# Kernel tuning notes

Hardware: AMD Instinct MI355X
Metric: run time of the kernel (lower is better)

The kernel has to match this reference:

```python
import jax, jax.numpy as jnp
import numpy as np

SEQ, B, XD, HD, ZD = 256, 128, 128, 1024, 64


def setup_inputs() -> dict:
    key = jax.random.key(0)
    ks = jax.random.split(key, 32)
    w = lambda k, shape: (jax.random.normal(k, shape, jnp.float32) * 0.02)
    inp = {
        "x": jax.random.uniform(ks[0], (SEQ, B, XD), jnp.float32),
        "eps": jax.random.normal(ks[1], (SEQ, B, ZD), jnp.float32),
        "phi_x_W": w(ks[2], (HD, XD)),   "phi_x_b": jnp.zeros((HD,), jnp.float32),
        "enc_W": w(ks[3], (HD, 2 * HD)), "enc_b": jnp.zeros((HD,), jnp.float32),
        "enc_mean_W": w(ks[4], (ZD, HD)), "enc_mean_b": jnp.zeros((ZD,), jnp.float32),
        "enc_std_W": w(ks[5], (ZD, HD)),  "enc_std_b": jnp.zeros((ZD,), jnp.float32),
        "prior_W": w(ks[6], (HD, HD)),   "prior_b": jnp.zeros((HD,), jnp.float32),
        "prior_mean_W": w(ks[7], (ZD, HD)), "prior_mean_b": jnp.zeros((ZD,), jnp.float32),
        "prior_std_W": w(ks[8], (ZD, HD)),  "prior_std_b": jnp.zeros((ZD,), jnp.float32),
        "phi_z_W": w(ks[9], (HD, ZD)),   "phi_z_b": jnp.zeros((HD,), jnp.float32),
        "dec1_W": w(ks[10], (HD, 2 * HD)), "dec1_b": jnp.zeros((HD,), jnp.float32),
        "dec2_W": w(ks[11], (XD, HD)),     "dec2_b": jnp.zeros((XD,), jnp.float32),
        "gru_Wi": w(ks[12], (3 * HD, 2 * HD)), "gru_Wh": w(ks[13], (3 * HD, HD)),
        "gru_bi": jnp.zeros((3 * HD,), jnp.float32), "gru_bh": jnp.zeros((3 * HD,), jnp.float32),
    }
    return inp


def _lin(x, W, b):
    return x @ W.T + b


def _vrnn(x, eps, phi_x_W, phi_x_b, enc_W, enc_b, enc_mean_W, enc_mean_b,
          enc_std_W, enc_std_b, prior_W, prior_b, prior_mean_W, prior_mean_b,
          prior_std_W, prior_std_b, phi_z_W, phi_z_b, dec1_W, dec1_b,
          dec2_W, dec2_b, gru_Wi, gru_Wh, gru_bi, gru_bh):
    batch = x.shape[1]
    h0 = jnp.zeros((batch, gru_Wh.shape[1]), x.dtype)

    def step(h, inp):
        x_t, eps_t = inp
        phi_x_t = jax.nn.relu(_lin(x_t, phi_x_W, phi_x_b))
        prior_t = jax.nn.relu(_lin(h, prior_W, prior_b))
        prior_mean_t = _lin(prior_t, prior_mean_W, prior_mean_b)
        prior_std_t = jnp.exp(0.5 * _lin(prior_t, prior_std_W, prior_std_b))
        enc_t = jax.nn.relu(_lin(jnp.concatenate([phi_x_t, h], axis=1), enc_W, enc_b))
        enc_mean_t = _lin(enc_t, enc_mean_W, enc_mean_b)
        enc_std_t = jnp.exp(0.5 * _lin(enc_t, enc_std_W, enc_std_b))
        z_t = enc_mean_t + eps_t * enc_std_t
        phi_z_t = jax.nn.relu(_lin(z_t, phi_z_W, phi_z_b))
        dec_h = jax.nn.relu(_lin(jnp.concatenate([phi_z_t, h], axis=1), dec1_W, dec1_b))
        logits_t = _lin(dec_h, dec2_W, dec2_b)  # sigmoid(logits) is the reconstruction
        # GRU cell (PyTorch gate ordering r, z, n)
        u_t = jnp.concatenate([phi_x_t, phi_z_t], axis=1)
        gi = _lin(u_t, gru_Wi, gru_bi)
        gh = _lin(h, gru_Wh, gru_bh)
        hd = h.shape[1]
        i_r, i_z, i_n = gi[:, :hd], gi[:, hd:2 * hd], gi[:, 2 * hd:]
        h_r, h_z, h_n = gh[:, :hd], gh[:, hd:2 * hd], gh[:, 2 * hd:]
        r = jax.nn.sigmoid(i_r + h_r)
        zg = jax.nn.sigmoid(i_z + h_z)
        n = jnp.tanh(i_n + r * h_n)
        h_new = (1.0 - zg) * n + zg * h
        # per-step losses (sum reduction, as in the torch code)
        # BCE(sigmoid(l), x) = x*softplus(-l) + (1-x)*softplus(l)
        recon_t = jnp.sum(x_t * jax.nn.softplus(-logits_t) + (1.0 - x_t) * jax.nn.softplus(logits_t))
        kld_t = -0.5 * jnp.sum(1.0 + 2.0 * jnp.log(enc_std_t)
                               - (enc_mean_t - prior_mean_t) ** 2
                               - (enc_std_t / prior_std_t) ** 2)
        return h_new, (logits_t, recon_t, kld_t)

    _, (logits, recon_ts, kld_ts) = jax.lax.scan(step, h0, (x, eps))
    recon_loss = jnp.sum(recon_ts) / batch
    kld_loss = jnp.sum(kld_ts) / batch
    x_recon = jax.nn.sigmoid(logits)
    return recon_loss, kld_loss, x_recon


def reference(x, eps, phi_x_W, phi_x_b, enc_W, enc_b, enc_mean_W, enc_mean_b,
              enc_std_W, enc_std_b, prior_W, prior_b, prior_mean_W, prior_mean_b,
              prior_std_W, prior_std_b, phi_z_W, phi_z_b, dec1_W, dec1_b,
              dec2_W, dec2_b, gru_Wi, gru_Wh, gru_bi, gru_bh):
    return _vrnn(x, eps, phi_x_W, phi_x_b, enc_W, enc_b, enc_mean_W, enc_mean_b,
                 enc_std_W, enc_std_b, prior_W, prior_b, prior_mean_W, prior_mean_b,
                 prior_std_W, prior_std_b, phi_z_W, phi_z_b, dec1_W, dec1_b,
                 dec2_W, dec2_b, gru_Wi, gru_Wh, gru_bi, gru_bh)
```

## Files before the change

### kernel.cpp

```cpp
#include <hip/hip_runtime.h>
#include <algorithm>

typedef __bf16 bf16;
typedef __bf16 bf16x8 __attribute__((ext_vector_type(8)));
typedef float f32x4 __attribute__((ext_vector_type(4)));
typedef unsigned long long u64;

#define SEQ 256
#define BATCH 128
#define XD 128
#define HD 1024
#define ZD 64
#define MROWS (SEQ * BATCH)
#define BH (BATCH * HD)
#define B3 (BATCH * 3072)
#define DYN_LDS 154432
#define NBLK 256

__device__ __forceinline__ f32x4 mfma16(bf16x8 a, bf16x8 b, f32x4 c) {
  return __builtin_amdgcn_mfma_f32_16x16x32_bf16(a, b, c, 0, 0, 0);
}
__device__ __forceinline__ float sigmoidf_(float x) { return 1.f / (1.f + __expf(-x)); }

__device__ __forceinline__ void cst16(bf16* p, bf16x8 v) {
  asm volatile("global_store_dwordx4 %0, %1, off sc0 sc1" ::"v"(p), "v"(v) : "memory");
}
__device__ __forceinline__ void cst16f(float* p, f32x4 v) {
  asm volatile("global_store_dwordx4 %0, %1, off sc0 sc1" ::"v"(p), "v"(v) : "memory");
}

__device__ __forceinline__ void gbar(unsigned* arr, unsigned* sum, unsigned serial) {
  asm volatile("s_waitcnt vmcnt(0) lgkmcnt(0)" ::: "memory");
  __syncthreads();
  const int tid = threadIdx.x;
  const int bid = blockIdx.x;
  if (tid == 0)
    __hip_atomic_store(arr + (size_t)bid * 32, serial, __ATOMIC_RELAXED,
                       __HIP_MEMORY_SCOPE_AGENT);
  if ((bid & 15) == 0 && tid < 16) {
    const unsigned* f = arr + (size_t)((bid & ~15) + tid) * 32;
    while (__hip_atomic_load(f, __ATOMIC_RELAXED, __HIP_MEMORY_SCOPE_AGENT) < serial)
      __builtin_amdgcn_s_sleep(2);
  }
  __syncthreads();
  if ((bid & 15) == 0 && tid == 0)
    __hip_atomic_store(sum + (size_t)(bid >> 4) * 32, serial, __ATOMIC_RELAXED,
                       __HIP_MEMORY_SCOPE_AGENT);
  if (tid < 16) {
    const unsigned* f = sum + (size_t)tid * 32;
    while (__hip_atomic_load(f, __ATOMIC_RELAXED, __HIP_MEMORY_SCOPE_AGENT) < serial)
      __builtin_amdgcn_s_sleep(2);
  }
  __builtin_amdgcn_fence(__ATOMIC_ACQUIRE, "agent");
  __syncthreads();
}

template <int MT, int NT>
__device__ __forceinline__ void mma_block(const bf16* __restrict__ a0, size_t aStride,
                                          const bf16* __restrict__ b0, size_t bStride,
                                          int K, f32x4 acc[MT][NT]) {
#pragma unroll 2
  for (int k = 0; k < K; k += 32) {
    bf16x8 af[MT], bfr[NT];
#pragma unroll
    for (int i = 0; i < MT; ++i) af[i] = *(const bf16x8*)(a0 + (size_t)i * aStride + k);
#pragma unroll
    for (int j = 0; j < NT; ++j) bfr[j] = *(const bf16x8*)(b0 + (size_t)j * bStride + k);
#pragma unroll
    for (int i = 0; i < MT; ++i)
#pragma unroll
      for (int j = 0; j < NT; ++j) acc[i][j] = mfma16(af[i], bfr[j], acc[i][j]);
  }
}

__global__ void cvt_k(bf16* __restrict__ dst, const float* __restrict__ src, long n,
                      int cols, int src_ld, int col_off) {
  long i = (long)blockIdx.x * blockDim.x + threadIdx.x;
  long stride = (long)gridDim.x * blockDim.x;
  for (; i < n; i += stride) {
    long row = i / cols;
    int c = (int)(i - row * cols);
    dst[i] = (bf16)src[row * (long)src_ld + col_off + c];
  }
}

struct Epi {
  bf16* C;
  float* Cf;
  const float* bias;
  const bf16* add;
  int relu;
  int ldc;
};

template <int MT, int NT>
__global__ void gemm_bt(const bf16* __restrict__ A, int lda, const bf16* __restrict__ B,
                        int ldb, int M, int N, int K, Epi e) {
  const int lane = threadIdx.x & 63;
  const int r = lane & 15, kb = lane >> 4;
  const int gw = blockIdx.x * (blockDim.x >> 6) + (threadIdx.x >> 6);
  const int nw = gridDim.x * (blockDim.x >> 6);
  const int ntm = M / (16 * MT), ntn = N / (16 * NT);
  for (int task = gw; task < ntm * ntn; task += nw) {
    int mt = task % ntm, nt = task / ntm;
    int m0 = mt * 16 * MT, n0 = nt * 16 * NT;
    f32x4 acc[MT][NT] = {};
    const bf16* a0 = A + (size_t)(m0 + r) * lda + kb * 8;
    const bf16* b0 = B + (size_t)(n0 + r) * ldb + kb * 8;
    mma_block<MT, NT>(a0, (size_t)16 * lda, b0, (size_t)16 * ldb, K, acc);
#pragma unroll
    for (int i = 0; i < MT; ++i)
#pragma unroll
      for (int j = 0; j < NT; ++j)
#pragma unroll
        for (int q = 0; q < 4; ++q) {
          size_t gm = (size_t)m0 + i * 16 + kb * 4 + q;
          int gn = n0 + j * 16 + r;
          float v = acc[i][j][q] + e.bias[gn];
          if (e.add) v += (float)e.add[gm * e.ldc + gn];
          if (e.relu) v = fmaxf(v, 0.f);
          if (e.Cf) e.Cf[gm * e.ldc + gn] = v;
          else e.C[gm * e.ldc + gn] = (bf16)v;
        }
  }
}

struct LoopP {
  const bf16 *WA, *WB, *WPZ, *WIZ, *WIX, *WXX, *WPX, *WDZ, *WD2, *XBF;
  bf16 *HB, *PT, *ET, *PHIX, *ENCX, *PHIZ, *DHP, *DECH;
  float *H, *GH, *GIX, *KLD, *RPART, *out;
  unsigned *ARR, *SUM, *PFLAG;
  const float *eps, *x;
  const float *prior_b, *gru_bh, *gru_bi, *pm_b, *ps_b, *em_b, *es_b, *pz_b, *phx_b,
      *enc_b, *dec1_b, *dec2_b;
};

__device__ __forceinline__ void stage1024(char* lds, int off, const bf16* src) {
  for (int c = threadIdx.x; c < 2048; c += 512) {
    int kg = c & 127, rr = c >> 7;
    *(float4*)(lds + off + (((kg << 4) + rr) << 4)) =
        *(const float4*)(src + (size_t)rr * 1024 + kg * 8);
  }
}

template <int KK>
__device__ __forceinline__ void load_af(bf16x8* af, const bf16* A, int row, int lda, int k0,
                                        int kb) {
#pragma unroll
  for (int kk = 0; kk < KK; ++kk)
    af[kk] = *(const bf16x8*)(A + (size_t)row * lda + k0 + kk * 32 + kb * 8);
}

template <int NU>
__device__ __forceinline__ void run_units(const bf16* Arow, const char* slab0, f32x4* acc,
                                          int r, int kb) {
  bf16x8 af[32];
#pragma unroll
  for (int kk = 0; kk < 32; ++kk) af[kk] = *(const bf16x8*)(Arow + kk * 32 + kb * 8);
#pragma unroll
  for (int u = 0; u < NU; ++u)
#pragma unroll
    for (int kk = 0; kk < 32; ++kk)
      acc[u] = mfma16(af[kk],
                      *(const bf16x8*)(slab0 + u * 32768 + ((((kk * 4 + kb) << 4) + r) << 4)),
                      acc[u]);
}

__device__ __forceinline__ void xpose2(float* wscr, const f32x4* acc, int ua, int r, int kb,
                                       int urow, int cb, int usel, float* vals) {
#pragma unroll
  for (int tdx = 0; tdx < 2; ++tdx) {
    f32x4 a = acc[ua + tdx];
    int base = tdx * 328 + (kb * 4) * 20 + r;
#pragma unroll
    for (int q = 0; q < 4; ++q) wscr[base + q * 20] = a[q];
  }
  asm volatile("s_waitcnt lgkmcnt(0)" ::: "memory");
  __builtin_amdgcn_sched_barrier(0);
  int rb = usel * 328 + urow * 20 + cb;
#pragma unroll
  for (int j = 0; j < 8; ++j) vals[j] = wscr[rb + j];
}

__global__ void __launch_bounds__(512, 1) vrnn_loop(LoopP p) {
  extern __shared__ char lds[];
  const int tid = threadIdx.x, lane = tid & 63, wv = tid >> 6;
  const int r = lane & 15, kb = lane >> 4;
  const int urow = (lane & 31) >> 1, cb = (lane & 1) * 8, usel = lane >> 5;
  const int b = blockIdx.x;
  unsigned bs = 0;

  int cls, uid0 = 0, gizj = 0, wpxb = 0;
  if (b < 8) cls = 0;
  else if (b < 104) { cls = 1; uid0 = 4 * (b - 8); }
  else if (b < 120) { cls = 2; uid0 = 4 * (b - 104); }
  else if (b < 122) { cls = 3; wpxb = b - 120; }
  else if (b < 186) { cls = 4; uid0 = 4 * (b - 122); }
  else if (b < 188) { cls = 5; uid0 = 4 * (b - 186); }
  else if (b < 252) { cls = 6; gizj = b - 188; }
  else cls = 7;

  float* wscr = (float*)(lds + 131072) + wv * 656;

  if (cls == 0) {
    for (int c = tid; c < 8192; c += 512) {
      int kg = c & 7, rr = (c >> 3) & 15, u = c >> 7;
      *(float4*)(lds + u * 2048 + (((kg << 4) + rr) << 4)) =
          *(const float4*)(p.WPZ + (size_t)(u * 16 + rr) * 64 + kg * 8);
    }
  } else if (cls == 1) {
    for (int u = 0; u < 4; ++u) stage1024(lds, u * 32768, p.WA + (size_t)(uid0 + u) * 16 * 1024);
  } else if (cls == 2) {
    for (int u = 0; u < 4; ++u) stage1024(lds, u * 32768, p.WDZ + (size_t)(uid0 + u) * 16 * 1024);
  } else if (cls == 3) {
    for (int c = tid; c < 8192; c += 512) {
      int u = c >> 8, kg = c & 15, rr = (c >> 4) & 15;
      *(float4*)(lds + u * 4096 + (((kg << 4) + rr) << 4)) =
          *(const float4*)(p.WPX + (size_t)((wpxb * 32 + u) * 16 + rr) * 128 + kg * 8);
    }
  } else if (cls == 4) {
    for (int u = 0; u < 4; ++u) {
      int uid = uid0 + u;
      const bf16* src = (uid < 64) ? p.WXX + (size_t)uid * 16 * 1024
                                   : p.WIX + (size_t)(uid - 64) * 16 * 1024;
      stage1024(lds, u * 32768, src);
    }
  } else if (cls == 5) {
    for (int u = 0; u < 4; ++u) stage1024(lds, u * 32768, p.WD2 + (size_t)(uid0 + u) * 16 * 1024);
  } else if (cls == 6) {
    for (int g = 0; g < 3; ++g)
      stage1024(lds, g * 32768, p.WIZ + (size_t)(g * 1024 + gizj * 16) * 1024);
  }
  __syncthreads();

  for (int t = 0; t < SEQ; ++t) {
    const int cur = t & 1, oth = cur ^ 1;

    if (cls == 1) {
      const bf16* Arow = p.HB + (size_t)(wv * 16 + r) * HD;
      f32x4 acc[4] = {};
      run_units<4>(Arow, lds, acc, r, kb);
#pragma unroll
      for (int up = 0; up < 4; up += 2) {
        float vals[8];
        xpose2(wscr, acc, up, r, kb, urow, cb, usel, vals);
        int uid = uid0 + up + usel;
        int gm = wv * 16 + urow;
        if (uid < 64) {
          int gn = uid * 16 + cb;
          bf16x8 o;
#pragma unroll
          for (int j = 0; j < 8; ++j) o[j] = (bf16)fmaxf(vals[j] + p.prior_b[gn + j], 0.f);
          cst16(&p.PT[gm * HD + gn], o);
        } else if (uid < 128) {
          int c = (uid - 64) * 16 + cb;
          bf16x8 ex = *(const bf16x8*)(p.ENCX + (size_t)cur * BH + gm * HD + c);
          bf16x8 o;
#pragma unroll
          for (int j = 0; j < 8; ++j) o[j] = (bf16)fmaxf(vals[j] + (float)ex[j], 0.f);
          cst16(&p.ET[gm * HD + c], o);
        } else if (uid < 320) {
          int c = (uid - 128) * 16 + cb;
          f32x4 g0, g1;
#pragma unroll
          for (int j = 0; j < 4; ++j) g0[j] = vals[j] + p.gru_bh[c + j];
#pragma unroll
          for (int j = 0; j < 4; ++j) g1[j] = vals[4 + j] + p.gru_bh[c + 4 + j];
          cst16f(&p.GH[gm * 3072 + c], g0);
          cst16f(&p.GH[gm * 3072 + c + 4], g1);
        } else {
          int c = (uid - 320) * 16 + cb;
          bf16x8 o;
#pragma unroll
          for (int j = 0; j < 8; ++j) o[j] = (bf16)vals[j];
          cst16(&p.DHP[(size_t)cur * BH + gm * HD + c], o);
        }
      }
    } else if (cls == 2 && t > 0) {
      const bf16* Arow = p.PHIZ + (size_t)oth * BH + (size_t)(wv * 16 + r) * HD;
      f32x4 acc[4] = {};
      run_units<4>(Arow, lds, acc, r, kb);
#pragma unroll
      for (int up = 0; up < 4; up += 2) {
        float vals[8];
        xpose2(wscr, acc, up, r, kb, urow, cb, usel, vals);
        int c = (uid0 + up + usel) * 16 + cb;
        int gm = wv * 16 + urow;
        bf16x8 dh = *(const bf16x8*)(p.DHP + (size_t)oth * BH + gm * HD + c);
        bf16x8 o;
#pragma unroll
        for (int j = 0; j < 8; ++j)
          o[j] = (bf16)fmaxf(vals[j] + (float)dh[j] + p.dec1_b[c + j], 0.f);
        cst16(&p.DECH[gm * HD + c], o);
      }
    } else if (cls == 3 && t < SEQ - 1) {
      bf16x8 af2[4];
      load_af<4>(af2, p.XBF + (size_t)(t + 1) * BATCH * XD, wv * 16 + r, 128, 0, kb);
#pragma unroll 1
      for (int up = 0; up < 32; up += 2) {
        f32x4 acc2[2] = {};
#pragma unroll
        for (int tdx = 0; tdx < 2; ++tdx)
#pragma unroll
          for (int kk = 0; kk < 4; ++kk)
            acc2[tdx] = mfma16(af2[kk],
                               *(const bf16x8*)(lds + (up + tdx) * 4096 +
                                                ((((kk * 4 + kb) << 4) + r) << 4)),
                               acc2[tdx]);
        float vals[8];
        xpose2(wscr, acc2, 0, r, kb, urow, cb, usel, vals);
        int gn = (wpxb * 32 + up + usel) * 16 + cb;
        int gm = wv * 16 + urow;
        bf16x8 o;
#pragma unroll
        for (int j = 0; j < 8; ++j) o[j] = (bf16)fmaxf(vals[j] + p.phx_b[gn + j], 0.f);
        cst16(&p.PHIX[gm * HD + gn], o);
      }
    }
    gbar(p.ARR, p.SUM, ++bs);

    if (cls == 0) {
      const int m0 = b * 16;
      const int mat = wv & 3, half = wv >> 2;
      float* sm = (float*)(lds + 131072);
      bf16* zs = (bf16*)(lds + 152064);
      float* red = (float*)(lds + 154368);
      {
        const bf16* Arow = ((mat < 2) ? p.PT : p.ET) + (size_t)(m0 + r) * HD;
        bf16x8 af[32];
#pragma unroll
        for (int kk = 0; kk < 32; ++kk) af[kk] = *(const bf16x8*)(Arow + kk * 32 + kb * 8);
        const float* bw = mat == 0 ? p.pm_b : mat == 1 ? p.ps_b : mat == 2 ? p.em_b : p.es_b;
#pragma unroll 1
        for (int nt = 0; nt < 2; ++nt) {
          int colb = half * 32 + nt * 16;
          f32x4 acc = {};
#pragma unroll
          for (int kk = 0; kk < 32; ++kk)
            acc = mfma16(af[kk],
                         *(const bf16x8*)(p.WB + (size_t)(mat * 64 + colb + r) * 1024 +
                                          kk * 32 + kb * 8),
                         acc);
#pragma unroll
          for (int qq = 0; qq < 4; ++qq)
            sm[mat * 1024 + (kb * 4 + qq) * 64 + colb + r] = acc[qq] + bw[colb + r];
        }
      }
      __syncthreads();
      float kacc = 0.f;
      for (int e = tid; e < 1024; e += 512) {
        int row = e >> 6, col = e & 63;
        float pm = sm[row * 64 + col], ps = sm[1024 + row * 64 + col];
        float em = sm[2048 + row * 64 + col], es = sm[3072 + row * 64 + col];
        float ev = p.eps[((size_t)t * BATCH + m0 + row) * ZD + col];
        zs[row * 72 + col] = (bf16)(em + ev * __expf(0.5f * es));
        float dm = em - pm;
        kacc += 1.f + es - dm * dm - __expf(es - ps);
      }
#pragma unroll
      for (int off = 32; off; off >>= 1) kacc += __shfl_down(kacc, off, 64);
      if (lane == 0) red[wv] = kacc;
      __syncthreads();
      if (tid == 0) {
        float ss = 0.f;
        for (int i = 0; i < 8; ++i) ss += red[i];
        p.KLD[t * 8 + b] = ss;
      }
      bf16x8 afz[2];
      afz[0] = *(const bf16x8*)(zs + r * 72 + kb * 8);
      afz[1] = *(const bf16x8*)(zs + r * 72 + 32 + kb * 8);
#pragma unroll 1
      for (int jp = 0; jp < 8; jp += 2) {
        f32x4 acc2[2] = {};
#pragma unroll
        for (int tdx = 0; tdx < 2; ++tdx) {
          int u = wv * 8 + jp + tdx;
#pragma unroll
          for (int kk = 0; kk < 2; ++kk)
            acc2[tdx] = mfma16(afz[kk],
                               *(const bf16x8*)(lds + u * 2048 +
                                                ((((kk * 4 + kb) << 4) + r) << 4)),
                               acc2[tdx]);
        }
        float vals[8];
        xpose2(wscr, acc2, 0, r, kb, urow, cb, usel, vals);
        int gn = (wv * 8 + jp + usel) * 16 + cb;
        int gm = m0 + urow;
        bf16x8 o;
#pragma unroll
        for (int j = 0; j < 8; ++j) o[j] = (bf16)fmaxf(vals[j] + p.pz_b[gn + j], 0.f);
        cst16(&p.PHIZ[(size_t)cur * BH + gm * HD + gn], o);
      }
      asm volatile("s_waitcnt vmcnt(0)" ::: "memory");
      __syncthreads();
      if (tid == 0)
        __hip_atomic_store(p.PFLAG + (size_t)b * 32, (unsigned)(t + 1), __ATOMIC_RELAXED,
                           __HIP_MEMORY_SCOPE_AGENT);
    } else if (cls == 4 && t < SEQ - 1) {
      const bf16* Arow = p.PHIX + (size_t)(wv * 16 + r) * HD;
      f32x4 acc[4] = {};
      run_units<4>(Arow, lds, acc, r, kb);
#pragma unroll
      for (int up = 0; up < 4; up += 2) {
        float vals[8];
        xpose2(wscr, acc, up, r, kb, urow, cb, usel, vals);
        int uid = uid0 + up + usel;
        int gm = wv * 16 + urow;
        if (uid < 64) {
          int c = uid * 16 + cb;
          bf16x8 o;
#pragma unroll
          for (int j = 0; j < 8; ++j) o[j] = (bf16)(vals[j] + p.enc_b[c + j]);
          cst16(&p.ENCX[(size_t)oth * BH + gm * HD + c], o);
        } else {
          int c = (uid - 64) * 16 + cb;
          f32x4 g0, g1;
#pragma unroll
          for (int j = 0; j < 4; ++j) g0[j] = vals[j] + p.gru_bi[c + j];
#pragma unroll
          for (int j = 0; j < 4; ++j) g1[j] = vals[4 + j] + p.gru_bi[c + 4 + j];
          cst16f(&p.GIX[(size_t)oth * B3 + gm * 3072 + c], g0);
          cst16f(&p.GIX[(size_t)oth * B3 + gm * 3072 + c + 4], g1);
        }
      }
    } else if (cls == 5 && t > 0) {
      const bf16* Arow = p.DECH + (size_t)(wv * 16 + r) * HD;
      f32x4 acc[4] = {};
      run_units<4>(Arow, lds, acc, r, kb);
      float racc = 0.f;
#pragma unroll
      for (int up = 0; up < 4; up += 2) {
        float vals[8];
        xpose2(wscr, acc, up, r, kb, urow, cb, usel, vals);
        int c = (uid0 + up + usel) * 16 + cb;
        int gm = wv * 16 + urow;
        size_t oi = ((size_t)(t - 1) * BATCH + gm) * XD + c;
#pragma unroll
        for (int j = 0; j < 8; ++j) {
          float l = vals[j] + p.dec2_b[c + j];
          p.out[2 + oi + j] = sigmoidf_(l);
          float spp = fmaxf(l, 0.f) + log1pf(__expf(-fabsf(l)));
          racc += spp - p.x[oi + j] * l;
        }
      }
#pragma unroll
      for (int off = 32; off; off >>= 1) racc += __shfl_down(racc, off, 64);
      if (lane == 0) p.RPART[(t - 1) * 64 + uid0 * 2 + wv] = racc;
    } else if (cls == 6) {
      if (tid < 8) {
        const unsigned* f = p.PFLAG + (size_t)tid * 32;
        while (__hip_atomic_load(f, __ATOMIC_RELAXED, __HIP_MEMORY_SCOPE_AGENT) <
               (unsigned)(t + 1))
          __builtin_amdgcn_s_sleep(1);
      }
      __syncthreads();
      __builtin_amdgcn_sched_barrier(0);
      float* scR = (float*)(lds + 98304);
      const int khalf = wv >> 2, mtg = wv & 3;
#pragma unroll 1
      for (int pass = 0; pass < 2; ++pass) {
        int mt = mtg + 4 * pass;
        const bf16* Arow = p.PHIZ + (size_t)cur * BH + (size_t)(mt * 16 + r) * HD;
        bf16x8 af[16];
#pragma unroll
        for (int kk = 0; kk < 16; ++kk)
          af[kk] = *(const bf16x8*)(Arow + khalf * 512 + kk * 32 + kb * 8);
        f32x4 a3[3] = {};
#pragma unroll
        for (int kk = 0; kk < 16; ++kk) {
          bf16x8 a = af[kk];
#pragma unroll
          for (int g = 0; g < 3; ++g)
            a3[g] = mfma16(a,
                           *(const bf16x8*)(lds + g * 32768 +
                                            (((((khalf * 16 + kk) * 4 + kb) << 4) + r) << 4)),
                           a3[g]);
        }
#pragma unroll
        for (int g = 0; g < 3; ++g)
#pragma unroll
          for (int q = 0; q < 4; ++q)
            scR[khalf * 3072 + mtg * 768 + g * 256 + (kb * 4 + q) * 16 + r] = a3[g][q];
        __syncthreads();
        if (tid < 128) {
          int mtg2 = tid >> 5, row = (tid & 31) >> 1, cb2 = (tid & 1) * 8;
          int gm = (mtg2 + 4 * pass) * 16 + row;
          int c = gizj * 16 + cb2;
          int base = mtg2 * 768 + row * 16 + cb2;
          float iv[3][8], hv[3][8];
#pragma unroll
          for (int g = 0; g < 3; ++g) {
            f32x4 i0 = *(const f32x4*)(p.GIX + (size_t)cur * B3 + gm * 3072 + g * 1024 + c);
            f32x4 i1 = *(const f32x4*)(p.GIX + (size_t)cur * B3 + gm * 3072 + g * 1024 + c + 4);
            f32x4 h0 = *(const f32x4*)(p.GH + gm * 3072 + g * 1024 + c);
            f32x4 h1 = *(const f32x4*)(p.GH + gm * 3072 + g * 1024 + c + 4);
#pragma unroll
            for (int j = 0; j < 8; ++j) {
              float part = scR[base + g * 256 + j] + scR[3072 + base + g * 256 + j];
              iv[g][j] = part + ((j < 4) ? i0[j] : i1[j - 4]);
              hv[g][j] = (j < 4) ? h0[j] : h1[j - 4];
            }
          }
          f32x4 hc0 = *(const f32x4*)(p.H + gm * HD + c);
          f32x4 hc1 = *(const f32x4*)(p.H + gm * HD + c + 4);
          f32x4 hn0, hn1;
          bf16x8 o;
#pragma unroll
          for (int j = 0; j < 8; ++j) {
            float rr2 = sigmoidf_(iv[0][j] + hv[0][j]);
            float zg = sigmoidf_(iv[1][j] + hv[1][j]);
            float nn = tanhf(iv[2][j] + rr2 * hv[2][j]);
            float hvv = (j < 4) ? hc0[j] : hc1[j - 4];
            float hnew = (1.f - zg) * nn + zg * hvv;
            if (j < 4) hn0[j] = hnew; else hn1[j - 4] = hnew;
            o[j] = (bf16)hnew;
          }
          *(f32x4*)(p.H + gm * HD + c) = hn0;
          *(f32x4*)(p.H + gm * HD + c + 4) = hn1;
          cst16(&p.HB[gm * HD + c], o);
        }
        __syncthreads();
      }
    }
    gbar(p.ARR, p.SUM, ++bs);
  }
}

__global__ void dec2_last(const bf16* __restrict__ A, const bf16* __restrict__ W,
                          const float* __restrict__ x, const float* __restrict__ b2,
                          float* __restrict__ out, float* __restrict__ rpart) {
  const int lane = threadIdx.x & 63;
  const int r = lane & 15, kb = lane >> 4;
  const int w = blockIdx.x * 4 + (threadIdx.x >> 6);
  const int m0 = (w & 7) * 16, n0 = (w >> 3) * 16;
  f32x4 acc[1][1] = {};
  const bf16* a0 = A + (size_t)(m0 + r) * HD + kb * 8;
  const bf16* b0 = W + (size_t)(n0 + r) * HD + kb * 8;
  mma_block<1, 1>(a0, 0, b0, (size_t)16 * HD, HD, acc);
  float racc = 0.f;
#pragma unroll
  for (int q = 0; q < 4; ++q) {
    int gm = m0 + kb * 4 + q, gn = n0 + r;
    float l = acc[0][0][q] + b2[gn];
    size_t oi = ((size_t)255 * BATCH + gm) * XD + gn;
    out[2 + oi] = sigmoidf_(l);
    float spp = fmaxf(l, 0.f) + log1pf(__expf(-fabsf(l)));
    racc += spp - x[oi] * l;
  }
#pragma unroll
  for (int off = 32; off; off >>= 1) racc += __shfl_down(racc, off, 64);
  if (lane == 0) rpart[255 * 64 + w] = racc;
}

__global__ void finalize_k(const float* __restrict__ rp, const float* __restrict__ kp,
                           float* __restrict__ out) {
  __shared__ float s[256];
  int tid = threadIdx.x;
  float a = 0.f;
  for (int i = tid; i < 256 * 64; i += 256) a += rp[i];
  s[tid] = a;
  __syncthreads();
  for (int off = 128; off > 0; off >>= 1) {
    if (tid < off) s[tid] += s[tid + off];
    __syncthreads();
  }
  if (tid == 0) out[0] = s[0] / (float)BATCH;
  __syncthreads();
  float bb = 0.f;
  for (int i = tid; i < 2048; i += 256) bb += kp[i];
  s[tid] = bb;
  __syncthreads();
  for (int off = 128; off > 0; off >>= 1) {
    if (tid < off) s[tid] += s[tid + off];
    __syncthreads();
  }
  if (tid == 0) out[1] = -0.5f * s[0] / (float)BATCH;
}

__global__ void sentinel_k(float* out) {
  if (threadIdx.x == 0) { out[0] = 1e9f; out[1] = 1e9f; }
}

extern "C" void kernel_launch(void* const* d_in, const int* in_sizes, int n_in, void* d_out,
                              int out_size, void* d_ws, size_t ws_size, hipStream_t stream) {
  const float* x = (const float*)d_in[0];
  const float* eps = (const float*)d_in[1];
  const float* phi_x_W = (const float*)d_in[2];
  const float* phi_x_b = (const float*)d_in[3];
  const float* enc_W = (const float*)d_in[4];
  const float* enc_b = (const float*)d_in[5];
  const float* enc_mean_W = (const float*)d_in[6];
  const float* enc_mean_b = (const float*)d_in[7];
  const float* enc_std_W = (const float*)d_in[8];
  const float* enc_std_b = (const float*)d_in[9];
  const float* prior_W = (const float*)d_in[10];
  const float* prior_b = (const float*)d_in[11];
  const float* prior_mean_W = (const float*)d_in[12];
  const float* prior_mean_b = (const float*)d_in[13];
  const float* prior_std_W = (const float*)d_in[14];
  const float* prior_std_b = (const float*)d_in[15];
  const float* phi_z_W = (const float*)d_in[16];
  const float* phi_z_b = (const float*)d_in[17];
  const float* dec1_W = (const float*)d_in[18];
  const float* dec1_b = (const float*)d_in[19];
  const float* dec2_W = (const float*)d_in[20];
  const float* dec2_b = (const float*)d_in[21];
  const float* gru_Wi = (const float*)d_in[22];
  const float* gru_Wh = (const float*)d_in[23];
  const float* gru_bi = (const float*)d_in[24];
  const float* gru_bh = (const float*)d_in[25];
  float* out = (float*)d_out;

  char* w = (char*)d_ws;
  auto carve = [&](size_t bytes) {
    char* pp = w;
    w += (bytes + 255) & ~(size_t)255;
    return pp;
  };
  bf16* WA = (bf16*)carve((size_t)6144 * HD * 2);
  bf16* WB = (bf16*)carve((size_t)256 * HD * 2);
  bf16* WPZ = (bf16*)carve((size_t)HD * ZD * 2);
  bf16* WIZ = (bf16*)carve((size_t)3072 * HD * 2);
  bf16* WIX = (bf16*)carve((size_t)3072 * HD * 2);
  bf16* WXX = (bf16*)carve((size_t)HD * HD * 2);
  bf16* WPX = (bf16*)carve((size_t)HD * XD * 2);
  bf16* WDZ = (bf16*)carve((size_t)HD * HD * 2);
  bf16* WD2 = (bf16*)carve((size_t)XD * HD * 2);
  bf16* XBF = (bf16*)carve((size_t)MROWS * XD * 2);
  float* H = (float*)carve((size_t)BH * 4);
  bf16* HB = (bf16*)carve((size_t)BH * 2);
  bf16* PT = (bf16*)carve((size_t)BH * 2);
  bf16* ET = (bf16*)carve((size_t)BH * 2);
  float* GH = (float*)carve((size_t)B3 * 4);
  bf16* PHIX = (bf16*)carve((size_t)BH * 2);
  bf16* ENCX = (bf16*)carve((size_t)2 * BH * 2);
  bf16* PHIZ = (bf16*)carve((size_t)2 * BH * 2);
  bf16* DHP = (bf16*)carve((size_t)2 * BH * 2);
  bf16* DECH = (bf16*)carve((size_t)BH * 2);
  float* GIX = (float*)carve((size_t)2 * B3 * 4);
  float* KLD = (float*)carve((size_t)SEQ * 8 * 4);
  float* RPART = (float*)carve((size_t)SEQ * 64 * 4);
  unsigned* ARR = (unsigned*)carve((size_t)NBLK * 32 * 4);
  unsigned* SUM = (unsigned*)carve((size_t)16 * 32 * 4);
  unsigned* PFLAG = (unsigned*)carve((size_t)8 * 32 * 4);
  if ((size_t)(w - (char*)d_ws) > ws_size) {
    sentinel_k<<<1, 64, 0, stream>>>(out);
    return;
  }

  auto cvt = [&](bf16* dst, const float* src, long n, int cols, int ld, int off) {
    int grid = (int)std::min((n + 255) / 256, (long)2048);
    cvt_k<<<grid, 256, 0, stream>>>(dst, src, n, cols, ld, off);
  };
  cvt(WA, prior_W, (long)HD * HD, HD, HD, 0);
  cvt(WA + (size_t)HD * HD, enc_W, (long)HD * HD, HD, 2 * HD, HD);
  cvt(WA + (size_t)2048 * HD, gru_Wh, (long)3072 * HD, HD, HD, 0);
  cvt(WA + (size_t)5120 * HD, dec1_W, (long)HD * HD, HD, 2 * HD, HD);
  cvt(WB, prior_mean_W, (long)ZD * HD, HD, HD, 0);
  cvt(WB + (size_t)64 * HD, prior_std_W, (long)ZD * HD, HD, HD, 0);
  cvt(WB + (size_t)128 * HD, enc_mean_W, (long)ZD * HD, HD, HD, 0);
  cvt(WB + (size_t)192 * HD, enc_std_W, (long)ZD * HD, HD, HD, 0);
  cvt(WPZ, phi_z_W, (long)HD * ZD, ZD, ZD, 0);
  cvt(WIZ, gru_Wi, (long)3072 * HD, HD, 2 * HD, HD);
  cvt(WIX, gru_Wi, (long)3072 * HD, HD, 2 * HD, 0);
  cvt(WXX, enc_W, (long)HD * HD, HD, 2 * HD, 0);
  cvt(WPX, phi_x_W, (long)HD * XD, XD, XD, 0);
  cvt(WDZ, dec1_W, (long)HD * HD, HD, 2 * HD, 0);
  cvt(WD2, dec2_W, (long)XD * HD, HD, HD, 0);
  cvt(XBF, x, (long)MROWS * XD, XD, XD, 0);

  hipMemsetAsync(H, 0, (size_t)BH * 4, stream);
  hipMemsetAsync(HB, 0, (size_t)BH * 2, stream);
  hipMemsetAsync(RPART, 0, (size_t)SEQ * 64 * 4, stream);
  hipMemsetAsync(ARR, 0, (size_t)NBLK * 32 * 4, stream);
  hipMemsetAsync(SUM, 0, (size_t)16 * 32 * 4, stream);
  hipMemsetAsync(PFLAG, 0, (size_t)8 * 32 * 4, stream);

  Epi e1{PHIX, nullptr, phi_x_b, nullptr, 1, HD};
  gemm_bt<2, 2><<<32, 256, 0, stream>>>(XBF, XD, WPX, XD, BATCH, HD, XD, e1);
  Epi e2{ENCX, nullptr, enc_b, nullptr, 0, HD};
  gemm_bt<2, 2><<<32, 256, 0, stream>>>(PHIX, HD, WXX, HD, BATCH, HD, HD, e2);
  Epi e3{nullptr, GIX, gru_bi, nullptr, 0, 3072};
  gemm_bt<2, 2><<<96, 256, 0, stream>>>(PHIX, HD, WIX, HD, BATCH, 3072, HD, e3);

  LoopP lp;
  lp.WA = WA; lp.WB = WB; lp.WPZ = WPZ; lp.WIZ = WIZ; lp.WIX = WIX; lp.WXX = WXX;
  lp.WPX = WPX; lp.WDZ = WDZ; lp.WD2 = WD2; lp.XBF = XBF;
  lp.HB = HB; lp.PT = PT; lp.ET = ET; lp.PHIX = PHIX; lp.ENCX = ENCX; lp.PHIZ = PHIZ;
  lp.DHP = DHP; lp.DECH = DECH;
  lp.H = H; lp.GH = GH; lp.GIX = GIX; lp.KLD = KLD; lp.RPART = RPART; lp.out = out;
  lp.ARR = ARR; lp.SUM = SUM; lp.PFLAG = PFLAG;
  lp.eps = eps; lp.x = x;
  lp.prior_b = prior_b; lp.gru_bh = gru_bh; lp.gru_bi = gru_bi;
  lp.pm_b = prior_mean_b; lp.ps_b = prior_std_b; lp.em_b = enc_mean_b; lp.es_b = enc_std_b;
  lp.pz_b = phi_z_b; lp.phx_b = phi_x_b; lp.enc_b = enc_b; lp.dec1_b = dec1_b;
  lp.dec2_b = dec2_b;

  hipFuncSetAttribute(reinterpret_cast<const void*>(vrnn_loop),
                      hipFuncAttributeMaxDynamicSharedMemorySize, DYN_LDS);
  void* args[] = {&lp};
  hipLaunchCooperativeKernel(reinterpret_cast<const void*>(vrnn_loop), dim3(NBLK), dim3(512),
                             args, DYN_LDS, stream);

  Epi e4{DECH, nullptr, dec1_b, DHP + (size_t)1 * BH, 1, HD};
  gemm_bt<2, 2><<<32, 256, 0, stream>>>(PHIZ + (size_t)1 * BH, HD, WDZ, HD, BATCH, HD, HD, e4);
  dec2_last<<<16, 256, 0, stream>>>(DECH, WD2, x, dec2_b, out, RPART);
  finalize_k<<<1, 256, 0, stream>>>(RPART, KLD, out);
}
```

Baseline: 20.99 ms.

## Replace grid-wide barriers with per-block dataflow flags in persistent VRNN loop

Removes the two hierarchical grid barriers per timestep. Each block class now waits only on flags posted by the specific producer blocks it depends on, and posts its own flag when its stage finishes. HB is double-buffered so blocks can drift partially across timesteps without overwriting state still being read. The idle blocks now return early. The cost is a fragile hand-coded dependency graph, where a wrong producer index or a WAR hazard would cause races or deadlock.

```diff
diff --git a/kernel.cpp b/kernel.cpp
--- a/kernel.cpp
+++ b/kernel.cpp
@@ -29,30 +29,20 @@
   asm volatile("global_store_dwordx4 %0, %1, off sc0 sc1" ::"v"(p), "v"(v) : "memory");
 }
 
-__device__ __forceinline__ void gbar(unsigned* arr, unsigned* sum, unsigned serial) {
-  asm volatile("s_waitcnt vmcnt(0) lgkmcnt(0)" ::: "memory");
+__device__ __forceinline__ void flagwait1(const unsigned* f, unsigned want) {
+  while (__hip_atomic_load(f, __ATOMIC_RELAXED, __HIP_MEMORY_SCOPE_AGENT) < want)
+    __builtin_amdgcn_s_sleep(1);
+}
+__device__ __forceinline__ void waitfence() {
   __syncthreads();
-  const int tid = threadIdx.x;
-  const int bid = blockIdx.x;
-  if (tid == 0)
-    __hip_atomic_store(arr + (size_t)bid * 32, serial, __ATOMIC_RELAXED,
-                       __HIP_MEMORY_SCOPE_AGENT);
-  if ((bid & 15) == 0 && tid < 16) {
-    const unsigned* f = arr + (size_t)((bid & ~15) + tid) * 32;
-    while (__hip_atomic_load(f, __ATOMIC_RELAXED, __HIP_MEMORY_SCOPE_AGENT) < serial)
-      __builtin_amdgcn_s_sleep(2);
-  }
+  __builtin_amdgcn_fence(__ATOMIC_ACQUIRE, "agent");
+  __builtin_amdgcn_sched_barrier(0);
+}
+__device__ __forceinline__ void postflag(unsigned* f, unsigned v) {
+  asm volatile("s_waitcnt vmcnt(0)" ::: "memory");
   __syncthreads();
-  if ((bid & 15) == 0 && tid == 0)
-    __hip_atomic_store(sum + (size_t)(bid >> 4) * 32, serial, __ATOMIC_RELAXED,
-                       __HIP_MEMORY_SCOPE_AGENT);
-  if (tid < 16) {
-    const unsigned* f = sum + (size_t)tid * 32;
-    while (__hip_atomic_load(f, __ATOMIC_RELAXED, __HIP_MEMORY_SCOPE_AGENT) < serial)
-      __builtin_amdgcn_s_sleep(2);
-  }
-  __builtin_amdgcn_fence(__ATOMIC_ACQUIRE, "agent");
-  __syncthreads();
+  if (threadIdx.x == 0)
+    __hip_atomic_store(f, v, __ATOMIC_RELAXED, __HIP_MEMORY_SCOPE_AGENT);
 }
 
 template <int MT, int NT>
@@ -129,7 +119,7 @@
   const bf16 *WA, *WB, *WPZ, *WIZ, *WIX, *WXX, *WPX, *WDZ, *WD2, *XBF;
   bf16 *HB, *PT, *ET, *PHIX, *ENCX, *PHIZ, *DHP, *DECH;
   float *H, *GH, *GIX, *KLD, *RPART, *out;
-  unsigned *ARR, *SUM, *PFLAG;
+  unsigned* FLG;
   const float *eps, *x;
   const float *prior_b, *gru_bh, *gru_bi, *pm_b, *ps_b, *em_b, *es_b, *pz_b, *phx_b,
       *enc_b, *dec1_b, *dec2_b;
@@ -188,7 +178,6 @@
   const int r = lane & 15, kb = lane >> 4;
   const int urow = (lane & 31) >> 1, cb = (lane & 1) * 8, usel = lane >> 5;
   const int b = blockIdx.x;
-  unsigned bs = 0;
 
   int cls, uid0 = 0, gizj = 0, wpxb = 0;
   if (b < 8) cls = 0;
@@ -198,9 +187,10 @@
   else if (b < 186) { cls = 4; uid0 = 4 * (b - 122); }
   else if (b < 188) { cls = 5; uid0 = 4 * (b - 186); }
   else if (b < 252) { cls = 6; gizj = b - 188; }
-  else cls = 7;
+  else return;
 
   float* wscr = (float*)(lds + 131072) + wv * 656;
+  unsigned* myflag = p.FLG + (size_t)b * 32;
 
   if (cls == 0) {
     for (int c = tid; c < 8192; c += 512) {
@@ -235,9 +225,15 @@
 
   for (int t = 0; t < SEQ; ++t) {
     const int cur = t & 1, oth = cur ^ 1;
+    const unsigned wt = (unsigned)t, wt1 = (unsigned)(t + 1);
 
     if (cls == 1) {
-      const bf16* Arow = p.HB + (size_t)(wv * 16 + r) * HD;
+      if (tid < 64) flagwait1(p.FLG + (size_t)(188 + tid) * 32, wt);
+      else if (tid < 128) flagwait1(p.FLG + (size_t)(122 + tid - 64) * 32, wt);
+      else if (tid < 136) flagwait1(p.FLG + (size_t)(tid - 128) * 32, wt);
+      else if (tid < 152) flagwait1(p.FLG + (size_t)(104 + tid - 136) * 32, wt);
+      waitfence();
+      const bf16* Arow = p.HB + (size_t)oth * BH + (size_t)(wv * 16 + r) * HD;
       f32x4 acc[4] = {};
       run_units<4>(Arow, lds, acc, r, kb);
 #pragma unroll
@@ -276,50 +272,63 @@
           cst16(&p.DHP[(size_t)cur * BH + gm * HD + c], o);
         }
       }
-    } else if (cls == 2 && t > 0) {
-      const bf16* Arow = p.PHIZ + (size_t)oth * BH + (size_t)(wv * 16 + r) * HD;
-      f32x4 acc[4] = {};
-      run_units<4>(Arow, lds, acc, r, kb);
-#pragma unroll
-      for (int up = 0; up < 4; up += 2) {
-        float vals[8];
-        xpose2(wscr, acc, up, r, kb, urow, cb, usel, vals);
-        int c = (uid0 + up + usel) * 16 + cb;
-        int gm = wv * 16 + urow;
-        bf16x8 dh = *(const bf16x8*)(p.DHP + (size_t)oth * BH + gm * HD + c);
-        bf16x8 o;
-#pragma unroll
-        for (int j = 0; j < 8; ++j)
-          o[j] = (bf16)fmaxf(vals[j] + (float)dh[j] + p.dec1_b[c + j], 0.f);
-        cst16(&p.DECH[gm * HD + c], o);
-      }
-    } else if (cls == 3 && t < SEQ - 1) {
-      bf16x8 af2[4];
-      load_af<4>(af2, p.XBF + (size_t)(t + 1) * BATCH * XD, wv * 16 + r, 128, 0, kb);
+      postflag(myflag, wt1);
+    } else if (cls == 2) {
+      if (tid < 8) flagwait1(p.FLG + (size_t)tid * 32, wt);
+      else if (tid < 24) flagwait1(p.FLG + (size_t)(88 + tid - 8) * 32, wt);
+      else if (tid < 26) flagwait1(p.FLG + (size_t)(186 + tid - 24) * 32, wt);
+      waitfence();
+      if (t > 0) {
+        const bf16* Arow = p.PHIZ + (size_t)oth * BH + (size_t)(wv * 16 + r) * HD;
+        f32x4 acc[4] = {};
+        run_units<4>(Arow, lds, acc, r, kb);
+#pragma unroll
+        for (int up = 0; up < 4; up += 2) {
+          float vals[8];
+          xpose2(wscr, acc, up, r, kb, urow, cb, usel, vals);
+          int c = (uid0 + up + usel) * 16 + cb;
+          int gm = wv * 16 + urow;
+          bf16x8 dh = *(const bf16x8*)(p.DHP + (size_t)oth * BH + gm * HD + c);
+          bf16x8 o;
+#pragma unroll
+          for (int j = 0; j < 8; ++j)
+            o[j] = (bf16)fmaxf(vals[j] + (float)dh[j] + p.dec1_b[c + j], 0.f);
+          cst16(&p.DECH[gm * HD + c], o);
+        }
+      }
+      postflag(myflag, wt1);
+    } else if (cls == 3) {
+      if (tid < 64) flagwait1(p.FLG + (size_t)(122 + tid) * 32, wt);
+      waitfence();
+      if (t < SEQ - 1) {
+        bf16x8 af2[4];
+        load_af<4>(af2, p.XBF + (size_t)(t + 1) * BATCH * XD, wv * 16 + r, 128, 0, kb);
 #pragma unroll 1
-      for (int up = 0; up < 32; up += 2) {
-        f32x4 acc2[2] = {};
-#pragma unroll
-        for (int tdx = 0; tdx < 2; ++tdx)
-#pragma unroll
-          for (int kk = 0; kk < 4; ++kk)
-            acc2[tdx] = mfma16(af2[kk],
-                               *(const bf16x8*)(lds + (up + tdx) * 4096 +
-                                                ((((kk * 4 + kb) << 4) + r) << 4)),
-                               acc2[tdx]);
-        float vals[8];
-        xpose2(wscr, acc2, 0, r, kb, urow, cb, usel, vals);
-        int gn = (wpxb * 32 + up + usel) * 16 + cb;
-        int gm = wv * 16 + urow;
-        bf16x8 o;
-#pragma unroll
-        for (int j = 0; j < 8; ++j) o[j] = (bf16)fmaxf(vals[j] + p.phx_b[gn + j], 0.f);
-        cst16(&p.PHIX[gm * HD + gn], o);
-      }
-    }
-    gbar(p.ARR, p.SUM, ++bs);
-
-    if (cls == 0) {
+        for (int up = 0; up < 32; up += 2) {
+          f32x4 acc2[2] = {};
+#pragma unroll
+          for (int tdx = 0; tdx < 2; ++tdx)
+#pragma unroll
+            for (int kk = 0; kk < 4; ++kk)
+              acc2[tdx] = mfma16(af2[kk],
+                                 *(const bf16x8*)(lds + (up + tdx) * 4096 +
+                                                  ((((kk * 4 + kb) << 4) + r) << 4)),
+                                 acc2[tdx]);
+          float vals[8];
+          xpose2(wscr, acc2, 0, r, kb, urow, cb, usel, vals);
+          int gn = (wpxb * 32 + up + usel) * 16 + cb;
+          int gm = wv * 16 + urow;
+          bf16x8 o;
+#pragma unroll
+          for (int j = 0; j < 8; ++j) o[j] = (bf16)fmaxf(vals[j] + p.phx_b[gn + j], 0.f);
+          cst16(&p.PHIX[gm * HD + gn], o);
+        }
+      }
+      postflag(myflag, wt1);
+    } else if (cls == 0) {
+      if (tid < 32) flagwait1(p.FLG + (size_t)(8 + tid) * 32, wt1);
+      else if (tid < 48) flagwait1(p.FLG + (size_t)(104 + tid - 32) * 32, wt);
+      waitfence();
       const int m0 = b * 16;
       const int mat = wv & 3, half = wv >> 2;
       float* sm = (float*)(lds + 131072);
@@ -391,70 +400,74 @@
         for (int j = 0; j < 8; ++j) o[j] = (bf16)fmaxf(vals[j] + p.pz_b[gn + j], 0.f);
         cst16(&p.PHIZ[(size_t)cur * BH + gm * HD + gn], o);
       }
-      asm volatile("s_waitcnt vmcnt(0)" ::: "memory");
-      __syncthreads();
-      if (tid == 0)
-        __hip_atomic_store(p.PFLAG + (size_t)b * 32, (unsigned)(t + 1), __ATOMIC_RELAXED,
-                           __HIP_MEMORY_SCOPE_AGENT);
-    } else if (cls == 4 && t < SEQ - 1) {
-      const bf16* Arow = p.PHIX + (size_t)(wv * 16 + r) * HD;
-      f32x4 acc[4] = {};
-      run_units<4>(Arow, lds, acc, r, kb);
-#pragma unroll
-      for (int up = 0; up < 4; up += 2) {
-        float vals[8];
-        xpose2(wscr, acc, up, r, kb, urow, cb, usel, vals);
-        int uid = uid0 + up + usel;
-        int gm = wv * 16 + urow;
-        if (uid < 64) {
-          int c = uid * 16 + cb;
-          bf16x8 o;
-#pragma unroll
-          for (int j = 0; j < 8; ++j) o[j] = (bf16)(vals[j] + p.enc_b[c + j]);
-          cst16(&p.ENCX[(size_t)oth * BH + gm * HD + c], o);
-        } else {
-          int c = (uid - 64) * 16 + cb;
-          f32x4 g0, g1;
-#pragma unroll
-          for (int j = 0; j < 4; ++j) g0[j] = vals[j] + p.gru_bi[c + j];
-#pragma unroll
-          for (int j = 0; j < 4; ++j) g1[j] = vals[4 + j] + p.gru_bi[c + 4 + j];
-          cst16f(&p.GIX[(size_t)oth * B3 + gm * 3072 + c], g0);
-          cst16f(&p.GIX[(size_t)oth * B3 + gm * 3072 + c + 4], g1);
-        }
-      }
-    } else if (cls == 5 && t > 0) {
-      const bf16* Arow = p.DECH + (size_t)(wv * 16 + r) * HD;
-      f32x4 acc[4] = {};
-      run_units<4>(Arow, lds, acc, r, kb);
-      float racc = 0.f;
-#pragma unroll
-      for (int up = 0; up < 4; up += 2) {
-        float vals[8];
-        xpose2(wscr, acc, up, r, kb, urow, cb, usel, vals);
-        int c = (uid0 + up + usel) * 16 + cb;
-        int gm = wv * 16 + urow;
-        size_t oi = ((size_t)(t - 1) * BATCH + gm) * XD + c;
-#pragma unroll
-        for (int j = 0; j < 8; ++j) {
-          float l = vals[j] + p.dec2_b[c + j];
-          p.out[2 + oi + j] = sigmoidf_(l);
-          float spp = fmaxf(l, 0.f) + log1pf(__expf(-fabsf(l)));
-          racc += spp - p.x[oi + j] * l;
-        }
-      }
-#pragma unroll
-      for (int off = 32; off; off >>= 1) racc += __shfl_down(racc, off, 64);
-      if (lane == 0) p.RPART[(t - 1) * 64 + uid0 * 2 + wv] = racc;
-    } else if (cls == 6) {
-      if (tid < 8) {
-        const unsigned* f = p.PFLAG + (size_t)tid * 32;
-        while (__hip_atomic_load(f, __ATOMIC_RELAXED, __HIP_MEMORY_SCOPE_AGENT) <
-               (unsigned)(t + 1))
-          __builtin_amdgcn_s_sleep(1);
-      }
-      __syncthreads();
-      __builtin_amdgcn_sched_barrier(0);
+      postflag(myflag, wt1);
+    } else if (cls == 4) {
+      if (tid < 2) flagwait1(p.FLG + (size_t)(120 + tid) * 32, wt1);
+      else if (tid < 18) flagwait1(p.FLG + (size_t)(24 + tid - 2) * 32, wt);
+      else if (tid < 82) flagwait1(p.FLG + (size_t)(188 + tid - 18) * 32, wt);
+      waitfence();
+      if (t < SEQ - 1) {
+        const bf16* Arow = p.PHIX + (size_t)(wv * 16 + r) * HD;
+        f32x4 acc[4] = {};
+        run_units<4>(Arow, lds, acc, r, kb);
+#pragma unroll
+        for (int up = 0; up < 4; up += 2) {
+          float vals[8];
+          xpose2(wscr, acc, up, r, kb, urow, cb, usel, vals);
+          int uid = uid0 + up + usel;
+          int gm = wv * 16 + urow;
+          if (uid < 64) {
+            int c = uid * 16 + cb;
+            bf16x8 o;
+#pragma unroll
+            for (int j = 0; j < 8; ++j) o[j] = (bf16)(vals[j] + p.enc_b[c + j]);
+            cst16(&p.ENCX[(size_t)oth * BH + gm * HD + c], o);
+          } else {
+            int c = (uid - 64) * 16 + cb;
+            f32x4 g0, g1;
+#pragma unroll
+            for (int j = 0; j < 4; ++j) g0[j] = vals[j] + p.gru_bi[c + j];
+#pragma unroll
+            for (int j = 0; j < 4; ++j) g1[j] = vals[4 + j] + p.gru_bi[c + 4 + j];
+            cst16f(&p.GIX[(size_t)oth * B3 + gm * 3072 + c], g0);
+            cst16f(&p.GIX[(size_t)oth * B3 + gm * 3072 + c + 4], g1);
+          }
+        }
+      }
+      postflag(myflag, wt1);
+    } else if (cls == 5) {
+      if (tid < 16) flagwait1(p.FLG + (size_t)(104 + tid) * 32, wt1);
+      waitfence();
+      if (t > 0) {
+        const bf16* Arow = p.DECH + (size_t)(wv * 16 + r) * HD;
+        f32x4 acc[4] = {};
+        run_units<4>(Arow, lds, acc, r, kb);
+        float racc = 0.f;
+#pragma unroll
+        for (int up = 0; up < 4; up += 2) {
+          float vals[8];
+          xpose2(wscr, acc, up, r, kb, urow, cb, usel, vals);
+          int c = (uid0 + up + usel) * 16 + cb;
+          int gm = wv * 16 + urow;
+          size_t oi = ((size_t)(t - 1) * BATCH + gm) * XD + c;
+#pragma unroll
+          for (int j = 0; j < 8; ++j) {
+            float l = vals[j] + p.dec2_b[c + j];
+            p.out[2 + oi + j] = sigmoidf_(l);
+            float spp = fmaxf(l, 0.f) + log1pf(__expf(-fabsf(l)));
+            racc += spp - p.x[oi + j] * l;
+          }
+        }
+#pragma unroll
+        for (int off = 32; off; off >>= 1) racc += __shfl_down(racc, off, 64);
+        if (lane == 0) p.RPART[(t - 1) * 64 + uid0 * 2 + wv] = racc;
+      }
+      postflag(myflag, wt1);
+    } else {
+      if (tid < 8) flagwait1(p.FLG + (size_t)tid * 32, wt1);
+      else if (tid < 56) flagwait1(p.FLG + (size_t)(40 + tid - 8) * 32, wt1);
+      else if (tid < 120) flagwait1(p.FLG + (size_t)(122 + tid - 56) * 32, wt);
+      waitfence();
       float* scR = (float*)(lds + 98304);
       const int khalf = wv >> 2, mtg = wv & 3;
 #pragma unroll 1
@@ -517,12 +530,12 @@
           }
           *(f32x4*)(p.H + gm * HD + c) = hn0;
           *(f32x4*)(p.H + gm * HD + c + 4) = hn1;
-          cst16(&p.HB[gm * HD + c], o);
+          cst16(&p.HB[(size_t)cur * BH + gm * HD + c], o);
         }
         __syncthreads();
       }
+      postflag(myflag, wt1);
     }
-    gbar(p.ARR, p.SUM, ++bs);
   }
 }
 
@@ -628,7 +641,7 @@
   bf16* WD2 = (bf16*)carve((size_t)XD * HD * 2);
   bf16* XBF = (bf16*)carve((size_t)MROWS * XD * 2);
   float* H = (float*)carve((size_t)BH * 4);
-  bf16* HB = (bf16*)carve((size_t)BH * 2);
+  bf16* HB = (bf16*)carve((size_t)2 * BH * 2);
   bf16* PT = (bf16*)carve((size_t)BH * 2);
   bf16* ET = (bf16*)carve((size_t)BH * 2);
   float* GH = (float*)carve((size_t)B3 * 4);
@@ -640,9 +653,7 @@
   float* GIX = (float*)carve((size_t)2 * B3 * 4);
   float* KLD = (float*)carve((size_t)SEQ * 8 * 4);
   float* RPART = (float*)carve((size_t)SEQ * 64 * 4);
-  unsigned* ARR = (unsigned*)carve((size_t)NBLK * 32 * 4);
-  unsigned* SUM = (unsigned*)carve((size_t)16 * 32 * 4);
-  unsigned* PFLAG = (unsigned*)carve((size_t)8 * 32 * 4);
+  unsigned* FLG = (unsigned*)carve((size_t)256 * 32 * 4);
   if ((size_t)(w - (char*)d_ws) > ws_size) {
     sentinel_k<<<1, 64, 0, stream>>>(out);
     return;
@@ -670,11 +681,9 @@
   cvt(XBF, x, (long)MROWS * XD, XD, XD, 0);
 
   hipMemsetAsync(H, 0, (size_t)BH * 4, stream);
-  hipMemsetAsync(HB, 0, (size_t)BH * 2, stream);
+  hipMemsetAsync(HB, 0, (size_t)2 * BH * 2, stream);
   hipMemsetAsync(RPART, 0, (size_t)SEQ * 64 * 4, stream);
-  hipMemsetAsync(ARR, 0, (size_t)NBLK * 32 * 4, stream);
-  hipMemsetAsync(SUM, 0, (size_t)16 * 32 * 4, stream);
-  hipMemsetAsync(PFLAG, 0, (size_t)8 * 32 * 4, stream);
+  hipMemsetAsync(FLG, 0, (size_t)256 * 32 * 4, stream);
 
   Epi e1{PHIX, nullptr, phi_x_b, nullptr, 1, HD};
   gemm_bt<2, 2><<<32, 256, 0, stream>>>(XBF, XD, WPX, XD, BATCH, HD, XD, e1);
@@ -689,7 +698,7 @@
   lp.HB = HB; lp.PT = PT; lp.ET = ET; lp.PHIX = PHIX; lp.ENCX = ENCX; lp.PHIZ = PHIZ;
   lp.DHP = DHP; lp.DECH = DECH;
   lp.H = H; lp.GH = GH; lp.GIX = GIX; lp.KLD = KLD; lp.RPART = RPART; lp.out = out;
-  lp.ARR = ARR; lp.SUM = SUM; lp.PFLAG = PFLAG;
+  lp.FLG = FLG;
   lp.eps = eps; lp.x = x;
   lp.prior_b = prior_b; lp.gru_bh = gru_bh; lp.gru_bi = gru_bi;
   lp.pm_b = prior_mean_b; lp.ps_b = prior_std_b; lp.em_b = enc_mean_b; lp.es_b = enc_std_b;
```

Result: faster. 19.03 ms (-9.4%).
